# Optimization experiments

Hardware: AMD Instinct MI355X
Metric: run time of the kernel (lower is better)

The kernel has to match this reference:

```python
import jax, jax.numpy as jnp
import numpy as np
from jax import lax

T, B, F, H = 1024, 64, 256, 512


def setup_inputs() -> dict:
    key = jax.random.key(0)
    k1, k2, k3, k4, k5 = jax.random.split(key, 5)
    stdv = 1.0 / np.sqrt(H)
    return {
        "x": jax.random.normal(k1, (T, B, F), dtype=jnp.float32),
        "W_ih": jax.random.uniform(k2, (H, F), minval=-stdv, maxval=stdv, dtype=jnp.float32),
        "W_hh": jax.random.uniform(k3, (2 * H, H), minval=-stdv, maxval=stdv, dtype=jnp.float32),
        "b_ih": jax.random.uniform(k4, (H,), minval=-stdv, maxval=stdv, dtype=jnp.float32),
        "b_hh": jax.random.uniform(k5, (2 * H,), minval=-stdv, maxval=stdv, dtype=jnp.float32),
    }


def reference(x, W_ih, W_hh, b_ih, b_hh):
    # x: [T, B, F] time-major. MGU (minimal gated unit) recurrence.
    h0 = jnp.zeros((x.shape[1], W_ih.shape[0]), dtype=x.dtype)

    def step(h, x_t):
        i_n = x_t @ W_ih.T + b_ih                      # [B, H]
        gh = h @ W_hh.T + b_hh                         # [B, 2H]
        h_f, h_n = jnp.split(gh, 2, axis=1)
        f = jax.nn.sigmoid(h_f)                        # forget gate
        n = jnp.tanh(i_n + f * h_n)                    # new gate
        h_new = n + (1.0 - f) * (h - n)                # = f*n + (1-f)*h
        return h_new, h_new

    _, outputs = lax.scan(step, h0, x)                 # [T, B, H]
    return outputs
```

## Files before the change

### kernel.cpp

```cpp
#include <hip/hip_runtime.h>

#define TT 1024
#define BB 64
#define FF 256
#define HH 512
#define HPAD 544

typedef short bf16x8 __attribute__((ext_vector_type(8)));
typedef float f32x4  __attribute__((ext_vector_type(4)));

__global__ __launch_bounds__(256) void in_gemm(
    const float* __restrict__ x, const float* __restrict__ Wih,
    const float* __restrict__ bih, float* __restrict__ io)
{
    __shared__ float xs[32][68];
    __shared__ float wst[64][68];

    const int bid = blockIdx.x;
    const int rb = bid >> 3, cb = bid & 7;
    const int m0 = rb * 32, n0 = cb * 64;
    const int t  = threadIdx.x;
    const int ti = t >> 4, tj = t & 15;

    float acc[2][4] = {{0.f,0.f,0.f,0.f},{0.f,0.f,0.f,0.f}};

    for (int k0 = 0; k0 < FF; k0 += 64) {
        {
            int flat = t * 8;
            int row = flat >> 6, col = flat & 63;
            const float* src = &x[(size_t)(m0 + row) * FF + k0 + col];
            float4 a = *(const float4*)&src[0];
            float4 b = *(const float4*)&src[4];
            *(float4*)&xs[row][col]     = a;
            *(float4*)&xs[row][col + 4] = b;
        }
        {
            int j  = t >> 2;
            int kk = (t & 3) * 16;
            const float* src = &Wih[(size_t)(n0 + j) * FF + k0 + kk];
            #pragma unroll
            for (int q = 0; q < 4; ++q) {
                float4 v = *(const float4*)&src[q * 4];
                wst[kk + q*4 + 0][j] = v.x;
                wst[kk + q*4 + 1][j] = v.y;
                wst[kk + q*4 + 2][j] = v.z;
                wst[kk + q*4 + 3][j] = v.w;
            }
        }
        __syncthreads();
        #pragma unroll
        for (int k = 0; k < 64; k += 4) {
            float4 xa = *(const float4*)&xs[ti][k];
            float4 xb = *(const float4*)&xs[ti + 16][k];
            #pragma unroll
            for (int q = 0; q < 4; ++q) {
                float4 wv = *(const float4*)&wst[k + q][tj * 4];
                float xav = (&xa.x)[q], xbv = (&xb.x)[q];
                acc[0][0] = fmaf(xav, wv.x, acc[0][0]);
                acc[0][1] = fmaf(xav, wv.y, acc[0][1]);
                acc[0][2] = fmaf(xav, wv.z, acc[0][2]);
                acc[0][3] = fmaf(xav, wv.w, acc[0][3]);
                acc[1][0] = fmaf(xbv, wv.x, acc[1][0]);
                acc[1][1] = fmaf(xbv, wv.y, acc[1][1]);
                acc[1][2] = fmaf(xbv, wv.z, acc[1][2]);
                acc[1][3] = fmaf(xbv, wv.w, acc[1][3]);
            }
        }
        __syncthreads();
    }

    float4 bv = *(const float4*)&bih[n0 + tj * 4];
    float4 r0 = make_float4(acc[0][0]+bv.x, acc[0][1]+bv.y, acc[0][2]+bv.z, acc[0][3]+bv.w);
    float4 r1 = make_float4(acc[1][0]+bv.x, acc[1][1]+bv.y, acc[1][2]+bv.z, acc[1][3]+bv.w);
    *(float4*)&io[(size_t)(m0 + ti)      * HH + n0 + tj * 4] = r0;
    *(float4*)&io[(size_t)(m0 + ti + 16) * HH + n0 + tj * 4] = r1;
}

__device__ __forceinline__ unsigned short f2bf(float x) {
    unsigned u = __float_as_uint(x);
    return (unsigned short)((u + 0x7FFFu + ((u >> 16) & 1u)) >> 16);
}

#define PB4(i) "+v"(Bfrag[(i)+0]), "+v"(Bfrag[(i)+1]), "+v"(Bfrag[(i)+2]), "+v"(Bfrag[(i)+3])

__global__ __launch_bounds__(512, 2) void mgu_rec(
    const float* __restrict__ Whh, const float* __restrict__ bhh,
    float* __restrict__ io, float* __restrict__ hbuf)
{
    const int bid = blockIdx.x;
    const int s   = bid >> 5;
    const int g   = bid & 31;
    const int c0  = g * 2;
    const int tid = threadIdx.x;
    const int w   = tid >> 6;
    const int l   = tid & 63;
    const int n   = l & 15;
    const int q   = l >> 4;

    __shared__ short hstb[2][2][HPAD];
    __shared__ float lds_pad[20480];
    if (tid == 0) { volatile float* vp = lds_pad; vp[0] = 0.f; }

    bf16x8 Bfrag[16];
    {
        const int grow = (n < 8) ? (s * 64 + 8 * w + n)
                                 : (512 + s * 64 + 8 * w + (n - 8));
        const float* src = &Whh[(size_t)grow * HH + 8 * q];
        #pragma unroll
        for (int kk = 0; kk < 16; ++kk) {
            bf16x8 f;
            #pragma unroll
            for (int j = 0; j < 8; ++j)
                f[j] = (short)f2bf(src[32 * kk + j]);
            Bfrag[kk] = f;
        }
    }
    asm volatile("" : PB4(0), PB4(4), PB4(8), PB4(12));

    const bool epi = (l < 8);
    float bfv = 0.f, bnv = 0.f, hprev0 = 0.f, hprev1 = 0.f;
    float in_c0 = 0.f, in_c1 = 0.f, in_n0 = 0.f, in_n1 = 0.f;
    size_t ob0 = 0, ob1 = 0;
    if (epi) {
        const int row = s * 64 + 8 * w + l;
        bfv = bhh[row];
        bnv = bhh[512 + row];
        ob0 = (size_t)(c0 + 0) * HH + row;
        ob1 = (size_t)(c0 + 1) * HH + row;
        in_n0 = io[ob0];
        in_n1 = io[ob1];
    }

    const int kb = w * 64;

    for (int t = 0; t < TT; ++t) {
        const int par = t & 1;
        in_c0 = in_n0; in_c1 = in_n1;

        float v0, v1;
        if (t > 0) {
            const int tr      = t - 1;
            const int slot_r  = tr & 3;
            const unsigned ep = (unsigned)(((tr >> 2) % 3) + 1);
            const float* b0 = &hbuf[(size_t)slot_r * BB * HH
                                    + (size_t)c0 * HH + kb + l];
            const float* b1 = b0 + HH;
            for (;;) {
                v0 = __hip_atomic_load(b0, __ATOMIC_RELAXED, __HIP_MEMORY_SCOPE_AGENT);
                v1 = __hip_atomic_load(b1, __ATOMIC_RELAXED, __HIP_MEMORY_SCOPE_AGENT);
                bool ok = ((__float_as_uint(v0) & 3u) == ep) &&
                          ((__float_as_uint(v1) & 3u) == ep);
                if (__all(ok)) break;
            }
        } else {
            v0 = 0.f; v1 = 0.f;
        }
        hstb[par][0][kb + l] = (short)f2bf(v0);
        hstb[par][1][kb + l] = (short)f2bf(v1);

        if (epi && t + 1 < TT) {
            in_n0 = io[ob0 + (size_t)(t + 1) * BB * HH];
            in_n1 = io[ob1 + (size_t)(t + 1) * BB * HH];
        }

        __syncthreads();

        f32x4 accE = {0.f, 0.f, 0.f, 0.f};
        f32x4 accO = {0.f, 0.f, 0.f, 0.f};
        const short* abase = &hstb[par][l & 1][8 * q];
        #pragma unroll
        for (int kk = 0; kk < 8; ++kk) {
            bf16x8 aE = *(const bf16x8*)&abase[64 * kk];
            bf16x8 aO = *(const bf16x8*)&abase[64 * kk + 32];
            accE = __builtin_amdgcn_mfma_f32_16x16x32_bf16(aE, Bfrag[2*kk+0], accE, 0, 0, 0);
            accO = __builtin_amdgcn_mfma_f32_16x16x32_bf16(aO, Bfrag[2*kk+1], accO, 0, 0, 0);
        }
        const float fOwn0 = accE[0] + accO[0];
        const float fOwn1 = accE[1] + accO[1];
        const float oth0 = __shfl_xor(fOwn0, 8, 64);
        const float oth1 = __shfl_xor(fOwn1, 8, 64);

        if (epi) {
            float fg0 = __builtin_amdgcn_rcpf(1.f + __expf(-(fOwn0 + bfv)));
            float e20 = __expf(2.f * (in_c0 + fg0 * (oth0 + bnv)));
            float nv0 = 1.f - 2.f * __builtin_amdgcn_rcpf(e20 + 1.f);
            float hn0 = nv0 + (1.f - fg0) * (hprev0 - nv0);
            float fg1 = __builtin_amdgcn_rcpf(1.f + __expf(-(fOwn1 + bfv)));
            float e21 = __expf(2.f * (in_c1 + fg1 * (oth1 + bnv)));
            float nv1 = 1.f - 2.f * __builtin_amdgcn_rcpf(e21 + 1.f);
            float hn1 = nv1 + (1.f - fg1) * (hprev1 - nv1);
            hprev0 = hn0; hprev1 = hn1;

            const unsigned ep = (unsigned)(((t >> 2) % 3) + 1);
            float ev0 = __uint_as_float((__float_as_uint(hn0) & ~3u) | ep);
            float ev1 = __uint_as_float((__float_as_uint(hn1) & ~3u) | ep);
            const size_t doff = (size_t)(t & 3) * BB * HH;
            __hip_atomic_store(&hbuf[doff + ob0], ev0, __ATOMIC_RELAXED,
                               __HIP_MEMORY_SCOPE_AGENT);
            __hip_atomic_store(&hbuf[doff + ob1], ev1, __ATOMIC_RELAXED,
                               __HIP_MEMORY_SCOPE_AGENT);
            io[ob0 + (size_t)t * BB * HH] = hn0;
            io[ob1 + (size_t)t * BB * HH] = hn1;
        }
    }
}

extern "C" void kernel_launch(void* const* d_in, const int* in_sizes, int n_in,
                              void* d_out, int out_size, void* d_ws, size_t ws_size,
                              hipStream_t stream)
{
    const float* x   = (const float*)d_in[0];
    const float* Wih = (const float*)d_in[1];
    const float* Whh = (const float*)d_in[2];
    const float* bih = (const float*)d_in[3];
    const float* bhh = (const float*)d_in[4];
    float* io = (float*)d_out;

    float* hbuf = (float*)d_ws;

    (void)hipMemsetAsync(d_ws, 0, 4 * BB * HH * 4, stream);

    in_gemm<<<dim3(16384), dim3(256), 0, stream>>>(x, Wih, bih, io);
    mgu_rec<<<dim3(256), dim3(512), 0, stream>>>(Whh, bhh, io, hbuf);
}
```

Baseline: 1.512 ms.

## Interleave two batch groups per block to overlap cross-block hidden-state waits

Each recurrent block now handles two independent batch-column pairs (A and B) instead of one, and the grid shrinks from 256 to 128 blocks. The hidden-state loads for one group are issued speculatively while the other group computes, and are checked against the epoch tag before falling back to the spin loop. This is meant to hide the global-memory polling latency between blocks behind MFMA and epilogue work. The cost is twice the serial work per block, fewer blocks in flight, and a stale speculative read that still needs a re-poll.

Result: slower. 2.237 ms (+47.9%).

```diff
diff --git a/kernel.cpp b/kernel.cpp
--- a/kernel.cpp
+++ b/kernel.cpp
@@ -88,17 +88,19 @@
     float* __restrict__ io, float* __restrict__ hbuf)
 {
     const int bid = blockIdx.x;
-    const int s   = bid >> 5;
-    const int g   = bid & 31;
-    const int c0  = g * 2;
+    const int s   = bid >> 4;
+    const int j   = bid & 15;
+    const int cA  = 2 * j;
+    const int cB  = 2 * j + 32;
     const int tid = threadIdx.x;
     const int w   = tid >> 6;
     const int l   = tid & 63;
     const int n   = l & 15;
     const int q   = l >> 4;
 
-    __shared__ short hstb[2][2][HPAD];
-    __shared__ float lds_pad[20480];
+    __shared__ short hstA[2][2][HPAD];
+    __shared__ short hstB[2][2][HPAD];
+    __shared__ float lds_pad[19456];
     if (tid == 0) { volatile float* vp = lds_pad; vp[0] = 0.f; }
 
     bf16x8 Bfrag[16];
@@ -110,97 +112,181 @@
         for (int kk = 0; kk < 16; ++kk) {
             bf16x8 f;
             #pragma unroll
-            for (int j = 0; j < 8; ++j)
-                f[j] = (short)f2bf(src[32 * kk + j]);
+            for (int jj = 0; jj < 8; ++jj)
+                f[jj] = (short)f2bf(src[32 * kk + jj]);
             Bfrag[kk] = f;
         }
     }
     asm volatile("" : PB4(0), PB4(4), PB4(8), PB4(12));
 
     const bool epi = (l < 8);
-    float bfv = 0.f, bnv = 0.f, hprev0 = 0.f, hprev1 = 0.f;
-    float in_c0 = 0.f, in_c1 = 0.f, in_n0 = 0.f, in_n1 = 0.f;
-    size_t ob0 = 0, ob1 = 0;
+    const int  row = s * 64 + 8 * w + l;
+    float bfv = 0.f, bnv = 0.f;
+    float hpA0 = 0.f, hpA1 = 0.f, hpB0 = 0.f, hpB1 = 0.f;
+    float icA0, icA1, icB0, icB1;
+    float inA0 = 0.f, inA1 = 0.f, inB0 = 0.f, inB1 = 0.f;
+    size_t oA0 = 0, oA1 = 0, oB0 = 0, oB1 = 0;
     if (epi) {
-        const int row = s * 64 + 8 * w + l;
         bfv = bhh[row];
         bnv = bhh[512 + row];
-        ob0 = (size_t)(c0 + 0) * HH + row;
-        ob1 = (size_t)(c0 + 1) * HH + row;
-        in_n0 = io[ob0];
-        in_n1 = io[ob1];
+        oA0 = (size_t)(cA + 0) * HH + row;  oA1 = oA0 + HH;
+        oB0 = (size_t)(cB + 0) * HH + row;  oB1 = oB0 + HH;
+        inA0 = io[oA0]; inA1 = io[oA1];
+        inB0 = io[oB0]; inB1 = io[oB1];
     }
 
     const int kb = w * 64;
+    float sA0 = 0.f, sA1 = 0.f;
+    float sB0 = 0.f, sB1 = 0.f;
 
     for (int t = 0; t < TT; ++t) {
         const int par = t & 1;
-        in_c0 = in_n0; in_c1 = in_n1;
-
-        float v0, v1;
-        if (t > 0) {
-            const int tr      = t - 1;
-            const int slot_r  = tr & 3;
-            const unsigned ep = (unsigned)(((tr >> 2) % 3) + 1);
-            const float* b0 = &hbuf[(size_t)slot_r * BB * HH
-                                    + (size_t)c0 * HH + kb + l];
-            const float* b1 = b0 + HH;
-            for (;;) {
-                v0 = __hip_atomic_load(b0, __ATOMIC_RELAXED, __HIP_MEMORY_SCOPE_AGENT);
-                v1 = __hip_atomic_load(b1, __ATOMIC_RELAXED, __HIP_MEMORY_SCOPE_AGENT);
-                bool ok = ((__float_as_uint(v0) & 3u) == ep) &&
-                          ((__float_as_uint(v1) & 3u) == ep);
-                if (__all(ok)) break;
-            }
-        } else {
-            v0 = 0.f; v1 = 0.f;
-        }
-        hstb[par][0][kb + l] = (short)f2bf(v0);
-        hstb[par][1][kb + l] = (short)f2bf(v1);
-
-        if (epi && t + 1 < TT) {
-            in_n0 = io[ob0 + (size_t)(t + 1) * BB * HH];
-            in_n1 = io[ob1 + (size_t)(t + 1) * BB * HH];
-        }
-
-        __syncthreads();
-
-        f32x4 accE = {0.f, 0.f, 0.f, 0.f};
-        f32x4 accO = {0.f, 0.f, 0.f, 0.f};
-        const short* abase = &hstb[par][l & 1][8 * q];
-        #pragma unroll
-        for (int kk = 0; kk < 8; ++kk) {
-            bf16x8 aE = *(const bf16x8*)&abase[64 * kk];
-            bf16x8 aO = *(const bf16x8*)&abase[64 * kk + 32];
-            accE = __builtin_amdgcn_mfma_f32_16x16x32_bf16(aE, Bfrag[2*kk+0], accE, 0, 0, 0);
-            accO = __builtin_amdgcn_mfma_f32_16x16x32_bf16(aO, Bfrag[2*kk+1], accO, 0, 0, 0);
-        }
-        const float fOwn0 = accE[0] + accO[0];
-        const float fOwn1 = accE[1] + accO[1];
-        const float oth0 = __shfl_xor(fOwn0, 8, 64);
-        const float oth1 = __shfl_xor(fOwn1, 8, 64);
-
-        if (epi) {
-            float fg0 = __builtin_amdgcn_rcpf(1.f + __expf(-(fOwn0 + bfv)));
-            float e20 = __expf(2.f * (in_c0 + fg0 * (oth0 + bnv)));
-            float nv0 = 1.f - 2.f * __builtin_amdgcn_rcpf(e20 + 1.f);
-            float hn0 = nv0 + (1.f - fg0) * (hprev0 - nv0);
-            float fg1 = __builtin_amdgcn_rcpf(1.f + __expf(-(fOwn1 + bfv)));
-            float e21 = __expf(2.f * (in_c1 + fg1 * (oth1 + bnv)));
-            float nv1 = 1.f - 2.f * __builtin_amdgcn_rcpf(e21 + 1.f);
-            float hn1 = nv1 + (1.f - fg1) * (hprev1 - nv1);
-            hprev0 = hn0; hprev1 = hn1;
-
-            const unsigned ep = (unsigned)(((t >> 2) % 3) + 1);
-            float ev0 = __uint_as_float((__float_as_uint(hn0) & ~3u) | ep);
-            float ev1 = __uint_as_float((__float_as_uint(hn1) & ~3u) | ep);
-            const size_t doff = (size_t)(t & 3) * BB * HH;
-            __hip_atomic_store(&hbuf[doff + ob0], ev0, __ATOMIC_RELAXED,
-                               __HIP_MEMORY_SCOPE_AGENT);
-            __hip_atomic_store(&hbuf[doff + ob1], ev1, __ATOMIC_RELAXED,
-                               __HIP_MEMORY_SCOPE_AGENT);
-            io[ob0 + (size_t)t * BB * HH] = hn0;
-            io[ob1 + (size_t)t * BB * HH] = hn1;
+        icA0 = inA0; icA1 = inA1; icB0 = inB0; icB1 = inB1;
+
+        {
+            float v0, v1;
+            if (t > 0) {
+                const int tr = t - 1;
+                const unsigned ep = (unsigned)(((tr >> 2) % 3) + 1);
+                bool ok = ((__float_as_uint(sA0) & 3u) == ep) &&
+                          ((__float_as_uint(sA1) & 3u) == ep);
+                if (__all(ok)) { v0 = sA0; v1 = sA1; }
+                else {
+                    const float* b0 = &hbuf[(size_t)(tr & 3) * BB * HH
+                                            + (size_t)cA * HH + kb + l];
+                    const float* b1 = b0 + HH;
+                    for (;;) {
+                        v0 = __hip_atomic_load(b0, __ATOMIC_RELAXED, __HIP_MEMORY_SCOPE_AGENT);
+                        v1 = __hip_atomic_load(b1, __ATOMIC_RELAXED, __HIP_MEMORY_SCOPE_AGENT);
+                        bool k2 = ((__float_as_uint(v0) & 3u) == ep) &&
+                                  ((__float_as_uint(v1) & 3u) == ep);
+                        if (__all(k2)) break;
+                    }
+                }
+            } else { v0 = 0.f; v1 = 0.f; }
+            hstA[par][0][kb + l] = (short)f2bf(v0);
+            hstA[par][1][kb + l] = (short)f2bf(v1);
+
+            __syncthreads();
+
+            if (t > 0) {
+                const int tr = t - 1;
+                const float* b0 = &hbuf[(size_t)(tr & 3) * BB * HH
+                                        + (size_t)cB * HH + kb + l];
+                sB0 = __hip_atomic_load(b0,      __ATOMIC_RELAXED, __HIP_MEMORY_SCOPE_AGENT);
+                sB1 = __hip_atomic_load(b0 + HH, __ATOMIC_RELAXED, __HIP_MEMORY_SCOPE_AGENT);
+            }
+            if (epi && t + 1 < TT) {
+                const size_t st = (size_t)(t + 1) * BB * HH;
+                inA0 = io[oA0 + st]; inA1 = io[oA1 + st];
+                inB0 = io[oB0 + st]; inB1 = io[oB1 + st];
+            }
+
+            f32x4 accE = {0.f,0.f,0.f,0.f}, accO = {0.f,0.f,0.f,0.f};
+            const short* abase = &hstA[par][l & 1][8 * q];
+            #pragma unroll
+            for (int kk = 0; kk < 8; ++kk) {
+                bf16x8 aE = *(const bf16x8*)&abase[64 * kk];
+                bf16x8 aO = *(const bf16x8*)&abase[64 * kk + 32];
+                accE = __builtin_amdgcn_mfma_f32_16x16x32_bf16(aE, Bfrag[2*kk+0], accE, 0, 0, 0);
+                accO = __builtin_amdgcn_mfma_f32_16x16x32_bf16(aO, Bfrag[2*kk+1], accO, 0, 0, 0);
+            }
+            const float f0 = accE[0] + accO[0];
+            const float f1 = accE[1] + accO[1];
+            const float o0 = __shfl_xor(f0, 8, 64);
+            const float o1 = __shfl_xor(f1, 8, 64);
+
+            if (epi) {
+                float fg0 = __builtin_amdgcn_rcpf(1.f + __expf(-(f0 + bfv)));
+                float e20 = __expf(2.f * (icA0 + fg0 * (o0 + bnv)));
+                float nv0 = 1.f - 2.f * __builtin_amdgcn_rcpf(e20 + 1.f);
+                float hn0 = nv0 + (1.f - fg0) * (hpA0 - nv0);
+                float fg1 = __builtin_amdgcn_rcpf(1.f + __expf(-(f1 + bfv)));
+                float e21 = __expf(2.f * (icA1 + fg1 * (o1 + bnv)));
+                float nv1 = 1.f - 2.f * __builtin_amdgcn_rcpf(e21 + 1.f);
+                float hn1 = nv1 + (1.f - fg1) * (hpA1 - nv1);
+                hpA0 = hn0; hpA1 = hn1;
+
+                const unsigned ep = (unsigned)(((t >> 2) % 3) + 1);
+                float ev0 = __uint_as_float((__float_as_uint(hn0) & ~3u) | ep);
+                float ev1 = __uint_as_float((__float_as_uint(hn1) & ~3u) | ep);
+                const size_t doff = (size_t)(t & 3) * BB * HH;
+                __hip_atomic_store(&hbuf[doff + oA0], ev0, __ATOMIC_RELAXED, __HIP_MEMORY_SCOPE_AGENT);
+                __hip_atomic_store(&hbuf[doff + oA1], ev1, __ATOMIC_RELAXED, __HIP_MEMORY_SCOPE_AGENT);
+                const size_t st = (size_t)t * BB * HH;
+                io[oA0 + st] = hn0;
+                io[oA1 + st] = hn1;
+            }
+        }
+
+        {
+            float v0, v1;
+            if (t > 0) {
+                const int tr = t - 1;
+                const unsigned ep = (unsigned)(((tr >> 2) % 3) + 1);
+                bool ok = ((__float_as_uint(sB0) & 3u) == ep) &&
+                          ((__float_as_uint(sB1) & 3u) == ep);
+                if (__all(ok)) { v0 = sB0; v1 = sB1; }
+                else {
+                    const float* b0 = &hbuf[(size_t)(tr & 3) * BB * HH
+                                            + (size_t)cB * HH + kb + l];
+                    const float* b1 = b0 + HH;
+                    for (;;) {
+                        v0 = __hip_atomic_load(b0, __ATOMIC_RELAXED, __HIP_MEMORY_SCOPE_AGENT);
+                        v1 = __hip_atomic_load(b1, __ATOMIC_RELAXED, __HIP_MEMORY_SCOPE_AGENT);
+                        bool k2 = ((__float_as_uint(v0) & 3u) == ep) &&
+                                  ((__float_as_uint(v1) & 3u) == ep);
+                        if (__all(k2)) break;
+                    }
+                }
+            } else { v0 = 0.f; v1 = 0.f; }
+            hstB[par][0][kb + l] = (short)f2bf(v0);
+            hstB[par][1][kb + l] = (short)f2bf(v1);
+
+            __syncthreads();
+
+            if (t + 1 < TT) {
+                const float* b0 = &hbuf[(size_t)(t & 3) * BB * HH
+                                        + (size_t)cA * HH + kb + l];
+                sA0 = __hip_atomic_load(b0,      __ATOMIC_RELAXED, __HIP_MEMORY_SCOPE_AGENT);
+                sA1 = __hip_atomic_load(b0 + HH, __ATOMIC_RELAXED, __HIP_MEMORY_SCOPE_AGENT);
+            }
+
+            f32x4 accE = {0.f,0.f,0.f,0.f}, accO = {0.f,0.f,0.f,0.f};
+            const short* abase = &hstB[par][l & 1][8 * q];
+            #pragma unroll
+            for (int kk = 0; kk < 8; ++kk) {
+                bf16x8 aE = *(const bf16x8*)&abase[64 * kk];
+                bf16x8 aO = *(const bf16x8*)&abase[64 * kk + 32];
+                accE = __builtin_amdgcn_mfma_f32_16x16x32_bf16(aE, Bfrag[2*kk+0], accE, 0, 0, 0);
+                accO = __builtin_amdgcn_mfma_f32_16x16x32_bf16(aO, Bfrag[2*kk+1], accO, 0, 0, 0);
+            }
+            const float f0 = accE[0] + accO[0];
+            const float f1 = accE[1] + accO[1];
+            const float o0 = __shfl_xor(f0, 8, 64);
+            const float o1 = __shfl_xor(f1, 8, 64);
+
+            if (epi) {
+                float fg0 = __builtin_amdgcn_rcpf(1.f + __expf(-(f0 + bfv)));
+                float e20 = __expf(2.f * (icB0 + fg0 * (o0 + bnv)));
+                float nv0 = 1.f - 2.f * __builtin_amdgcn_rcpf(e20 + 1.f);
+                float hn0 = nv0 + (1.f - fg0) * (hpB0 - nv0);
+                float fg1 = __builtin_amdgcn_rcpf(1.f + __expf(-(f1 + bfv)));
+                float e21 = __expf(2.f * (icB1 + fg1 * (o1 + bnv)));
+                float nv1 = 1.f - 2.f * __builtin_amdgcn_rcpf(e21 + 1.f);
+                float hn1 = nv1 + (1.f - fg1) * (hpB1 - nv1);
+                hpB0 = hn0; hpB1 = hn1;
+
+                const unsigned ep = (unsigned)(((t >> 2) % 3) + 1);
+                float ev0 = __uint_as_float((__float_as_uint(hn0) & ~3u) | ep);
+                float ev1 = __uint_as_float((__float_as_uint(hn1) & ~3u) | ep);
+                const size_t doff = (size_t)(t & 3) * BB * HH;
+                __hip_atomic_store(&hbuf[doff + oB0], ev0, __ATOMIC_RELAXED, __HIP_MEMORY_SCOPE_AGENT);
+                __hip_atomic_store(&hbuf[doff + oB1], ev1, __ATOMIC_RELAXED, __HIP_MEMORY_SCOPE_AGENT);
+                const size_t st = (size_t)t * BB * HH;
+                io[oB0 + st] = hn0;
+                io[oB1 + st] = hn1;
+            }
         }
     }
 }
@@ -221,5 +307,5 @@
     (void)hipMemsetAsync(d_ws, 0, 4 * BB * HH * 4, stream);
 
     in_gemm<<<dim3(16384), dim3(256), 0, stream>>>(x, Wih, bih, io);
-    mgu_rec<<<dim3(256), dim3(512), 0, stream>>>(Whh, bhh, io, hbuf);
+    mgu_rec<<<dim3(128), dim3(512), 0, stream>>>(Whh, bhh, io, hbuf);
 }
```

## Rewrite input projection GEMM with split-bf16 MFMA instead of FP32 FMA

Applied to the files above, without the earlier changes.

The input projection x@W_ih^T moves from an LDS-tiled FP32 FMA kernel to MFMA bf16 instructions. Each operand is split into hi and lo bf16 parts, and three MFMAs are issued per tile to keep close to FP32 accuracy. Each block now computes 32 rows by all 512 columns and loads operands straight from global memory without LDS. This cuts the grid from 16384 to 2048 blocks. The GEMM is a small share next to the 1024-step recurrence, so the total gain is limited, and the uncoalesced scalar output stores and repeated W_ih conversion add overhead.

New measurement: 1.433 ms. -5.2%, faster.

```diff
diff --git a/kernel.cpp b/kernel.cpp
--- a/kernel.cpp
+++ b/kernel.cpp
@@ -9,76 +9,96 @@
 typedef short bf16x8 __attribute__((ext_vector_type(8)));
 typedef float f32x4  __attribute__((ext_vector_type(4)));
 
+__device__ __forceinline__ unsigned short f2bf(float x) {
+    unsigned u = __float_as_uint(x);
+    return (unsigned short)((u + 0x7FFFu + ((u >> 16) & 1u)) >> 16);
+}
+__device__ __forceinline__ float bf2f(unsigned short h) {
+    return __uint_as_float(((unsigned)h) << 16);
+}
+
 __global__ __launch_bounds__(256) void in_gemm(
     const float* __restrict__ x, const float* __restrict__ Wih,
     const float* __restrict__ bih, float* __restrict__ io)
 {
-    __shared__ float xs[32][68];
-    __shared__ float wst[64][68];
-
-    const int bid = blockIdx.x;
-    const int rb = bid >> 3, cb = bid & 7;
-    const int m0 = rb * 32, n0 = cb * 64;
-    const int t  = threadIdx.x;
-    const int ti = t >> 4, tj = t & 15;
-
-    float acc[2][4] = {{0.f,0.f,0.f,0.f},{0.f,0.f,0.f,0.f}};
-
-    for (int k0 = 0; k0 < FF; k0 += 64) {
-        {
-            int flat = t * 8;
-            int row = flat >> 6, col = flat & 63;
-            const float* src = &x[(size_t)(m0 + row) * FF + k0 + col];
-            float4 a = *(const float4*)&src[0];
-            float4 b = *(const float4*)&src[4];
-            *(float4*)&xs[row][col]     = a;
-            *(float4*)&xs[row][col + 4] = b;
-        }
-        {
-            int j  = t >> 2;
-            int kk = (t & 3) * 16;
-            const float* src = &Wih[(size_t)(n0 + j) * FF + k0 + kk];
-            #pragma unroll
-            for (int q = 0; q < 4; ++q) {
-                float4 v = *(const float4*)&src[q * 4];
-                wst[kk + q*4 + 0][j] = v.x;
-                wst[kk + q*4 + 1][j] = v.y;
-                wst[kk + q*4 + 2][j] = v.z;
-                wst[kk + q*4 + 3][j] = v.w;
-            }
-        }
-        __syncthreads();
-        #pragma unroll
-        for (int k = 0; k < 64; k += 4) {
-            float4 xa = *(const float4*)&xs[ti][k];
-            float4 xb = *(const float4*)&xs[ti + 16][k];
-            #pragma unroll
-            for (int q = 0; q < 4; ++q) {
-                float4 wv = *(const float4*)&wst[k + q][tj * 4];
-                float xav = (&xa.x)[q], xbv = (&xb.x)[q];
-                acc[0][0] = fmaf(xav, wv.x, acc[0][0]);
-                acc[0][1] = fmaf(xav, wv.y, acc[0][1]);
-                acc[0][2] = fmaf(xav, wv.z, acc[0][2]);
-                acc[0][3] = fmaf(xav, wv.w, acc[0][3]);
-                acc[1][0] = fmaf(xbv, wv.x, acc[1][0]);
-                acc[1][1] = fmaf(xbv, wv.y, acc[1][1]);
-                acc[1][2] = fmaf(xbv, wv.z, acc[1][2]);
-                acc[1][3] = fmaf(xbv, wv.w, acc[1][3]);
-            }
-        }
-        __syncthreads();
-    }
-
-    float4 bv = *(const float4*)&bih[n0 + tj * 4];
-    float4 r0 = make_float4(acc[0][0]+bv.x, acc[0][1]+bv.y, acc[0][2]+bv.z, acc[0][3]+bv.w);
-    float4 r1 = make_float4(acc[1][0]+bv.x, acc[1][1]+bv.y, acc[1][2]+bv.z, acc[1][3]+bv.w);
-    *(float4*)&io[(size_t)(m0 + ti)      * HH + n0 + tj * 4] = r0;
-    *(float4*)&io[(size_t)(m0 + ti + 16) * HH + n0 + tj * 4] = r1;
-}
-
-__device__ __forceinline__ unsigned short f2bf(float x) {
-    unsigned u = __float_as_uint(x);
-    return (unsigned short)((u + 0x7FFFu + ((u >> 16) & 1u)) >> 16);
+    const int m0   = blockIdx.x * 32;
+    const int tid  = threadIdx.x;
+    const int w    = tid >> 6;
+    const int l    = tid & 63;
+    const int rowA = l & 15;
+    const int koff = 8 * (l >> 4);
+
+    f32x4 acc[2][8];
+    #pragma unroll
+    for (int mt = 0; mt < 2; ++mt)
+        #pragma unroll
+        for (int nt = 0; nt < 8; ++nt)
+            acc[mt][nt] = (f32x4){0.f, 0.f, 0.f, 0.f};
+
+    #pragma unroll 1
+    for (int kk = 0; kk < 8; ++kk) {
+        bf16x8 Ahi[2], Alo[2];
+        #pragma unroll
+        for (int mt = 0; mt < 2; ++mt) {
+            const float* ax = &x[(size_t)(m0 + mt * 16 + rowA) * FF + 32 * kk + koff];
+            float4 a0 = *(const float4*)&ax[0];
+            float4 a1 = *(const float4*)&ax[4];
+            float av[8] = {a0.x, a0.y, a0.z, a0.w, a1.x, a1.y, a1.z, a1.w};
+            bf16x8 h, lo;
+            #pragma unroll
+            for (int j = 0; j < 8; ++j) {
+                unsigned short hb = f2bf(av[j]);
+                h[j]  = (short)hb;
+                lo[j] = (short)f2bf(av[j] - bf2f(hb));
+            }
+            Ahi[mt] = h; Alo[mt] = lo;
+        }
+        #pragma unroll
+        for (int half = 0; half < 2; ++half) {
+            bf16x8 Bhi[4], Blo[4];
+            #pragma unroll
+            for (int n4 = 0; n4 < 4; ++n4) {
+                const int ncol = 128 * w + (half * 4 + n4) * 16 + rowA;
+                const float* bw = &Wih[(size_t)ncol * FF + 32 * kk + koff];
+                float4 b0 = *(const float4*)&bw[0];
+                float4 b1 = *(const float4*)&bw[4];
+                float bv[8] = {b0.x, b0.y, b0.z, b0.w, b1.x, b1.y, b1.z, b1.w};
+                bf16x8 h, lo;
+                #pragma unroll
+                for (int j = 0; j < 8; ++j) {
+                    unsigned short hb = f2bf(bv[j]);
+                    h[j]  = (short)hb;
+                    lo[j] = (short)f2bf(bv[j] - bf2f(hb));
+                }
+                Bhi[n4] = h; Blo[n4] = lo;
+            }
+            #pragma unroll
+            for (int mt = 0; mt < 2; ++mt)
+                #pragma unroll
+                for (int n4 = 0; n4 < 4; ++n4) {
+                    const int nt = half * 4 + n4;
+                    f32x4 a = acc[mt][nt];
+                    a = __builtin_amdgcn_mfma_f32_16x16x32_bf16(Ahi[mt], Bhi[n4], a, 0, 0, 0);
+                    a = __builtin_amdgcn_mfma_f32_16x16x32_bf16(Alo[mt], Bhi[n4], a, 0, 0, 0);
+                    a = __builtin_amdgcn_mfma_f32_16x16x32_bf16(Ahi[mt], Blo[n4], a, 0, 0, 0);
+                    acc[mt][nt] = a;
+                }
+        }
+    }
+
+    #pragma unroll
+    for (int nt = 0; nt < 8; ++nt) {
+        const int col = 128 * w + nt * 16 + rowA;
+        const float bv = bih[col];
+        #pragma unroll
+        for (int mt = 0; mt < 2; ++mt) {
+            #pragma unroll
+            for (int r = 0; r < 4; ++r) {
+                const int row = m0 + mt * 16 + (l >> 4) * 4 + r;
+                io[(size_t)row * HH + col] = acc[mt][nt][r] + bv;
+            }
+        }
+    }
 }
 
 #define PB4(i) "+v"(Bfrag[(i)+0]), "+v"(Bfrag[(i)+1]), "+v"(Bfrag[(i)+2]), "+v"(Bfrag[(i)+3])
@@ -220,6 +240,6 @@
 
     (void)hipMemsetAsync(d_ws, 0, 4 * BB * HH * 4, stream);
 
-    in_gemm<<<dim3(16384), dim3(256), 0, stream>>>(x, Wih, bih, io);
+    in_gemm<<<dim3(2048), dim3(256), 0, stream>>>(x, Wih, bih, io);
     mgu_rec<<<dim3(256), dim3(512), 0, stream>>>(Whh, bhh, io, hbuf);
 }
```
